# Performance work log

Measured on AMD Instinct MI355X. Metric: run time of the kernel, lower is better.

The kernel has to match this reference:

```python
import jax, jax.numpy as jnp
import numpy as np

B, N, K, CIN, COUT, H = 4, 2048, 32, 16, 32, 32
EPS = 1e-5


def setup_inputs() -> dict:
    key = jax.random.key(0)
    ks = jax.random.split(key, 6)
    s = 0.1
    return dict(
        xyz=jax.random.uniform(ks[0], (B, N, 3), dtype=jnp.float32),
        points=jax.random.normal(ks[1], (B, N, CIN), dtype=jnp.float32),
        W1=jax.random.normal(ks[2], (3, H), dtype=jnp.float32) * s,
        b1=jnp.zeros((H,), jnp.float32),
        g1=jnp.ones((H,), jnp.float32),
        be1=jnp.zeros((H,), jnp.float32),
        W2=jax.random.normal(ks[3], (H, H), dtype=jnp.float32) * s,
        b2=jnp.zeros((H,), jnp.float32),
        g2=jnp.ones((H,), jnp.float32),
        be2=jnp.zeros((H,), jnp.float32),
        W3=jax.random.normal(ks[4], (H, CIN * COUT), dtype=jnp.float32) * s,
        b3=jnp.zeros((CIN * COUT,), jnp.float32),
        gbn=jnp.ones((COUT,), jnp.float32),
        bbn=jnp.zeros((COUT,), jnp.float32),
    )


def _bn(h, g, b):
    # BatchNorm1d training-mode math: biased batch stats over axis 0
    return g * (h - h.mean(0)) / jnp.sqrt(h.var(0) + EPS) + b


def reference(xyz, points, W1, b1, g1, be1, W2, b2, g2, be2, W3, b3, gbn, bbn):
    # KNN: squared distances (B,N,N)
    sq = jnp.sum(xyz * xyz, -1)
    dist = -2.0 * jnp.einsum('bmc,bnc->bmn', xyz, xyz) + sq[:, :, None] + sq[:, None, :]
    _, idx = jax.lax.top_k(-dist, K)  # (B,N,K) nearest neighbors

    gather = jax.vmap(lambda p, i: p[i])  # (N,C),(N,K)->(N,K,C), vmapped over B
    grouped_xyz = gather(xyz, idx)                      # (B,N,K,3)
    rel = grouped_xyz - xyz[:, :, None, :]              # (B,N,K,3)
    grouped_pts = gather(points, idx)                   # (B,N,K,CIN)

    # weight net on relative coords
    h = rel.reshape(-1, 3)
    h = _bn(jax.nn.relu(h @ W1 + b1), g1, be1)
    h = _bn(jax.nn.relu(h @ W2 + b2), g2, be2)
    w = (h @ W3 + b3).reshape(B, N, K, CIN, COUT)       # (B,N,K,CIN,COUT)

    # weighted sum over C_in, then max over neighbors
    out = jnp.einsum('bnkc,bnkco->bnko', grouped_pts, w)  # (B,N,K,COUT)
    out = out.max(axis=2)                                 # (B,N,COUT)

    # final BatchNorm1d over (B,N) per channel
    m = out.mean((0, 1))
    v = out.var((0, 1))
    return gbn * (out - m) / jnp.sqrt(v + EPS) + bbn
```

## Files before the change

### kernel.cpp

```cpp
#include <hip/hip_runtime.h>

#define B_ 4
#define N_ 2048
#define K_ 32
#define CIN_ 16
#define COUT_ 32
#define H_ 32
#define R_ (B_*N_*K_)
#define EPS_ 1e-5f
#define INVR_ (1.0f/(float)R_)
#define INVBN_ (1.0f/(float)(B_*N_))
#define LISTCAP 192
#define NSH 16

typedef __attribute__((ext_vector_type(8)))  _Float16 f16x8;
typedef __attribute__((ext_vector_type(2)))  __fp16   hw16x2;
typedef __attribute__((ext_vector_type(2)))  _Float16 f16x2;
typedef __attribute__((ext_vector_type(16))) float    f32x16;

__device__ __forceinline__ float dot3f(float ax,float ay,float az,float bx,float by,float bz){
    return fmaf(az,bz, fmaf(ay,by, ax*bx));
}
__device__ __forceinline__ unsigned int flip_f32(float d){
    unsigned int u = __float_as_uint(d);
    return u ^ ((unsigned int)(((int)u) >> 31) | 0x80000000u);
}
__device__ __forceinline__ unsigned int pk2(float a, float b){
    union { hw16x2 v; unsigned int u; } c;
    c.v = __builtin_amdgcn_cvt_pkrtz(a, b);
    return c.u;
}
__device__ __forceinline__ unsigned int pkmul(unsigned int a, unsigned int b){
    union { unsigned int u; f16x2 v; } x, y, r;
    x.u = a; y.u = b; r.v = x.v * y.v; return r.u;
}
__device__ __forceinline__ float shsum(const float* __restrict__ p, int k){
    float s = 0.f;
    #pragma unroll
    for (int i = 0; i < NSH; ++i) s += p[i*32 + k];
    return s;
}

__device__ __forceinline__ void hsel4(const unsigned int* hq , int lane,
                                      unsigned int Kthr, int* Bsel, unsigned int* below){
    unsigned int g[4];
    #pragma unroll
    for (int t = 0; t < 4; ++t){
        uint4 h = ((const uint4*)hq)[4*lane + t];
        g[t] = h.x + h.y + h.z + h.w;
    }
    unsigned int gs = g[0]+g[1]+g[2]+g[3], cum = gs;
    #pragma unroll
    for (int off = 1; off < 64; off <<= 1){
        unsigned int v = __shfl_up(cum, off);
        if (lane >= off) cum += v;
    }
    unsigned long long bal = __ballot(cum >= Kthr);
    int L = __ffsll(bal) - 1;
    unsigned int run = __shfl(cum, L) - __shfl(gs, L);
    unsigned int h0 = __shfl(g[0], L), h1 = __shfl(g[1], L), h2 = __shfl(g[2], L);
    if      (run + h0 >= Kthr)           { *Bsel = 4*L;     *below = run; }
    else if (run + h0 + h1 >= Kthr)      { *Bsel = 4*L + 1; *below = run + h0; }
    else if (run + h0 + h1 + h2 >= Kthr) { *Bsel = 4*L + 2; *below = run + h0 + h1; }
    else                                 { *Bsel = 4*L + 3; *below = run + h0 + h1 + h2; }
}

__global__ __launch_bounds__(256) void k_prep0(const float* __restrict__ xyz, float4* __restrict__ xs4g,
                                               float* __restrict__ st){
    int i = blockIdx.x*256 + threadIdx.x;
    float x = xyz[3*i], y = xyz[3*i+1], z = xyz[3*i+2];
    xs4g[i] = make_float4(x, y, z, dot3f(x,y,z,x,y,z));
    if (blockIdx.x == 0){
        for (int j = threadIdx.x; j < 1152; j += 256) st[j] = 0.f;
    }
}

__global__ __launch_bounds__(256,4) void k_knn(const float4* __restrict__ xs4g,
                                               const float* __restrict__ W1, const float* __restrict__ b1,
                                               int* __restrict__ idx_out,
                                               float* __restrict__ s1sh, float* __restrict__ q1sh){
    __shared__ uint4 hist4[4][256];
    __shared__ unsigned long long lst[4][LISTCAP];
    __shared__ int kidx[4][K_];

    const int tid  = threadIdx.x;
    const int w    = tid >> 6;
    const int lane = tid & 63;
    const int half = lane >> 5;
    const int b    = blockIdx.x >> 9;
    const int q    = ((blockIdx.x & 511) << 2) + w;
    const int bN   = b * N_;
    unsigned int* hw = (unsigned int*)hist4[w];

    const uint4 z4 = make_uint4(0,0,0,0);
    hist4[w][lane] = z4; hist4[w][64+lane] = z4; hist4[w][128+lane] = z4; hist4[w][192+lane] = z4;

    const float4 qp = xs4g[bN + q];
    const float qx = qp.x, qy = qp.y, qz = qp.z, sqq = qp.w;

    unsigned int fv[32];
    #pragma unroll
    for (int j = 0; j < 32; ++j){
        int c = j*64 + lane;
        float4 pt = xs4g[bN + c];
        float d = fmaf(-2.0f, dot3f(qx,qy,qz, pt.x,pt.y,pt.z), sqq) + pt.w;
        unsigned int f = flip_f32(d);
        fv[j] = f;
        atomicAdd(&hw[(f >> 24)*4 + (lane & 3)], 1u);
    }
    int B0; unsigned int lt0;
    hsel4(hw, lane, (unsigned)K_, &B0, &lt0);
    unsigned int Kp = (unsigned)K_ - lt0;

    hist4[w][lane] = z4; hist4[w][64+lane] = z4; hist4[w][128+lane] = z4; hist4[w][192+lane] = z4;
    #pragma unroll
    for (int j = 0; j < 32; ++j){
        if ((int)(fv[j] >> 24) == B0)
            atomicAdd(&hw[((fv[j] >> 16) & 0xFF)*4 + (lane & 3)], 1u);
    }
    int B1s; unsigned int lt1;
    hsel4(hw, lane, Kp, &B1s, &lt1);

    const unsigned long long mlt = (lane == 63) ? ~0ull >> 1 : (1ull << lane) - 1ull;
    unsigned int cnt = 0;
    #pragma unroll
    for (int j = 0; j < 32; ++j){
        unsigned int f = fv[j];
        int top = (int)(f >> 24);
        bool surv = (top < B0) || (top == B0 && (int)((f >> 16) & 0xFF) <= B1s);
        unsigned long long sb = __ballot(surv);
        unsigned int pos = cnt + (unsigned int)__popcll(sb & mlt);
        if (surv && pos < (unsigned)LISTCAP)
            lst[w][pos] = ((unsigned long long)f << 32) | (unsigned int)(j*64 + lane);
        cnt += (unsigned int)__popcll(sb);
    }
    int m = (int)cnt; if (m > LISTCAP) m = LISTCAP;

    int* outp = idx_out + ((size_t)bN + q) * K_;
    for (int i = lane; i < m; i += 64){
        unsigned long long my = lst[w][i];
        int rank = 0;
        for (int jj = 0; jj < m; ++jj)
            rank += (lst[w][jj] < my) ? 1 : 0;
        if (rank < K_){
            int id = (int)(unsigned int)(my & 0xFFFFFFFFull);
            outp[rank] = id;
            kidx[w][rank] = id;
        }
    }

    {
        const int ch = lane & 31;
        float w1a = W1[ch], w1b = W1[H_+ch], w1c = W1[2*H_+ch], b1c = b1[ch];
        float s = 0.f, qq = 0.f;
        #pragma unroll
        for (int r = 0; r < 16; ++r){
            int idr = kidx[w][half*16 + r];
            float4 pn = xs4g[bN + idr];
            float rx = pn.x - qx, ry = pn.y - qy, rz = pn.z - qz;
            float h = fmaxf(fmaf(rx, w1a, fmaf(ry, w1b, fmaf(rz, w1c, b1c))), 0.0f);
            s += h; qq = fmaf(h, h, qq);
        }
        s  += __shfl_xor(s, 32, 64);
        qq += __shfl_xor(qq, 32, 64);
        if (lane < 32){
            int sh = (blockIdx.x & (NSH-1)) * 32 + ch;
            atomicAdd(&s1sh[sh], s);
            atomicAdd(&q1sh[sh], qq);
        }
    }
}

__device__ __forceinline__ void compute_h1v(const float4* __restrict__ xs4g, const int* __restrict__ idx, int r,
                                            const float* __restrict__ W1, const float* __restrict__ b1, float* h1){
    int b = r >> 16;
    int n = (r >> 5) & (N_-1);
    int id = idx[r];
    float4 pc = xs4g[b*N_ + n];
    float4 pn = xs4g[b*N_ + id];
    float rx = pn.x - pc.x, ry = pn.y - pc.y, rz = pn.z - pc.z;
    #pragma unroll
    for (int j = 0; j < H_; ++j){
        float a = fmaf(rx, W1[j], fmaf(ry, W1[H_+j], fmaf(rz, W1[2*H_+j], b1[j])));
        h1[j] = fmaxf(a, 0.0f);
    }
}

__global__ __launch_bounds__(256) void k_prep2(const float* __restrict__ points,
                                               const float* __restrict__ s1s, const float* __restrict__ q1s,
                                               const float* __restrict__ g1, const float* __restrict__ be1,
                                               const float* __restrict__ W2, const float* __restrict__ b2,
                                               unsigned int* __restrict__ pf16, unsigned int* __restrict__ W2f,
                                               float* __restrict__ b2p){
    int flat = blockIdx.x*256 + threadIdx.x;
    if (flat < 65536){
        pf16[flat] = pk2(points[2*flat], points[2*flat+1]);
    } else if (flat < 66048){
        int d = flat - 65536;
        int jj = d & 3, lane = (d >> 2) & 63, s = d >> 8;
        int col = lane & 31;
        int k0 = s*16 + (lane >> 5)*8 + 2*jj;
        float m0 = shsum(s1s,k0)*INVR_,   v0 = shsum(q1s,k0)*INVR_   - m0*m0;
        float m1 = shsum(s1s,k0+1)*INVR_, v1 = shsum(q1s,k0+1)*INVR_ - m1*m1;
        float a0  = g1[k0]   / sqrtf(v0 + EPS_);
        float a1v = g1[k0+1] / sqrtf(v1 + EPS_);
        W2f[d] = pk2(a0*W2[k0*H_ + col], a1v*W2[(k0+1)*H_ + col]);
    } else if (flat < 66080){
        int col = flat - 66048;
        float acc = b2[col];
        #pragma unroll 4
        for (int h = 0; h < H_; ++h){
            float mm = shsum(s1s,h)*INVR_, vv = shsum(q1s,h)*INVR_ - mm*mm;
            float aa = g1[h] / sqrtf(vv + EPS_);
            float bb = fmaf(-aa, mm, be1[h]);
            acc = fmaf(bb, W2[h*H_ + col], acc);
        }
        b2p[col] = acc;
    }
}

__global__ __launch_bounds__(256,3) void k_h2stats(const float4* __restrict__ xs4g, const int* __restrict__ idx,
                                                   const float* __restrict__ W1, const float* __restrict__ b1,
                                                   const uint4* __restrict__ W2f, const float* __restrict__ b2p,
                                                   float* gsum, float* gsq){
    __shared__ float redS[H_], redQ[H_];
    const int tid = threadIdx.x, lane = tid & 63, w = tid >> 6;
    const int half = lane >> 5, m = lane & 31;
    if (tid < H_){ redS[tid] = 0.f; redQ[tid] = 0.f; }
    __syncthreads();

    int r = blockIdx.x*256 + tid;
    float h1[H_];
    compute_h1v(xs4g, idx, r, W1, b1, h1);
    unsigned int h1p[16];
    #pragma unroll
    for (int i = 0; i < 16; ++i) h1p[i] = pk2(h1[2*i], h1[2*i+1]);

    union { uint4 u4; f16x8 v; } Bf0, Bf1;
    Bf0.u4 = W2f[lane];
    Bf1.u4 = W2f[64 + lane];
    float b2c = b2p[m];

    float s = 0.f, q = 0.f;
    #pragma unroll
    for (int t = 0; t < 2; ++t){
        const int src = t*32 + m;
        union { unsigned int u[4]; f16x8 v; } a0, a1f;
        #pragma unroll
        for (int jj = 0; jj < 4; ++jj){
            unsigned int lo = __shfl(h1p[jj],     src, 64);
            unsigned int hi = __shfl(h1p[4 + jj], src, 64);
            a0.u[jj] = half ? hi : lo;
        }
        #pragma unroll
        for (int jj = 0; jj < 4; ++jj){
            unsigned int lo = __shfl(h1p[8 + jj],  src, 64);
            unsigned int hi = __shfl(h1p[12 + jj], src, 64);
            a1f.u[jj] = half ? hi : lo;
        }
        f32x16 acc;
        #pragma unroll
        for (int i = 0; i < 16; ++i) acc[i] = b2c;
        acc = __builtin_amdgcn_mfma_f32_32x32x16_f16(a0.v,  Bf0.v, acc, 0, 0, 0);
        acc = __builtin_amdgcn_mfma_f32_32x32x16_f16(a1f.v, Bf1.v, acc, 0, 0, 0);
        #pragma unroll
        for (int i = 0; i < 16; ++i){
            float v = fmaxf(acc[i], 0.0f);
            s += v; q = fmaf(v, v, q);
        }
    }
    s += __shfl_xor(s, 32, 64);
    q += __shfl_xor(q, 32, 64);
    if (lane < 32){ atomicAdd(&redS[m], s); atomicAdd(&redQ[m], q); }
    __syncthreads();
    if (tid < H_){ atomicAdd(&gsum[tid], redS[tid]); atomicAdd(&gsq[tid], redQ[tid]); }
}

__global__ __launch_bounds__(256) void k_prep3(const float* __restrict__ W3, const float* __restrict__ b3,
                                               const float* __restrict__ s2, const float* __restrict__ q2,
                                               const float* __restrict__ g2, const float* __restrict__ be2,
                                               unsigned int* __restrict__ W3f){
    int d = blockIdx.x*256 + threadIdx.x;
    int jj = d & 3, lane = (d >> 2) & 63, step = d >> 8;
    int col = lane & 31;
    int off = (lane >> 5)*8 + 2*jj;
    float v0, v1;
    if (step < 32){
        int h = step, c0 = off;
        float mm = s2[h]*INVR_, vv = q2[h]*INVR_ - mm*mm;
        float aa = g2[h] / sqrtf(vv + EPS_);
        v0 = aa * W3[h*512 + c0*COUT_ + col];
        v1 = aa * W3[h*512 + (c0+1)*COUT_ + col];
    } else {
        int c0 = off;
        v0 = b3[c0*COUT_ + col]; v1 = b3[(c0+1)*COUT_ + col];
        #pragma unroll 4
        for (int h = 0; h < H_; ++h){
            float mm = s2[h]*INVR_, vv = q2[h]*INVR_ - mm*mm;
            float aa = g2[h] / sqrtf(vv + EPS_);
            float bb = fmaf(-aa, mm, be2[h]);
            v0 = fmaf(bb, W3[h*512 + c0*COUT_ + col], v0);
            v1 = fmaf(bb, W3[h*512 + (c0+1)*COUT_ + col], v1);
        }
    }
    W3f[d] = pk2(v0, v1);
}

__global__ __launch_bounds__(256,3) void k_out(const float4* __restrict__ xs4g, const int* __restrict__ idx,
                                               const float* __restrict__ W1, const float* __restrict__ b1,
                                               const uint4* __restrict__ W2f, const float* __restrict__ b2p,
                                               const unsigned int* __restrict__ pf16,
                                               const uint4* __restrict__ W3f,
                                               float* __restrict__ out_pre, float* gsum, float* gsq){
    __shared__ float redS[COUT_], redQ[COUT_];
    const int tid = threadIdx.x, lane = tid & 63, w = tid >> 6;
    const int half = lane >> 5, m = lane & 31;
    if (tid < COUT_){ redS[tid] = 0.f; redQ[tid] = 0.f; }
    __syncthreads();

    const int rB = blockIdx.x*256 + w*64;
    int r = blockIdx.x*256 + tid;

    float h1[H_];
    compute_h1v(xs4g, idx, r, W1, b1, h1);
    unsigned int h1p[16];
    #pragma unroll
    for (int i = 0; i < 16; ++i) h1p[i] = pk2(h1[2*i], h1[2*i+1]);

    union { uint4 u4; f16x8 v; } A0, A1;
    A0.u4 = W2f[lane];
    A1.u4 = W2f[64 + lane];
    float b2v[16];
    #pragma unroll
    for (int i = 0; i < 16; ++i) b2v[i] = b2p[(i&3) + 8*(i>>2) + 4*half];

    const uint4* Wf = W3f + lane;

    #pragma unroll
    for (int t = 0; t < 2; ++t){
        const int src = t*32 + m;
        union { unsigned int u[4]; f16x8 v; } B0f, B1f;
        #pragma unroll
        for (int jj = 0; jj < 4; ++jj){
            unsigned int lo = __shfl(h1p[jj],     src, 64);
            unsigned int hi = __shfl(h1p[4 + jj], src, 64);
            B0f.u[jj] = half ? hi : lo;
        }
        #pragma unroll
        for (int jj = 0; jj < 4; ++jj){
            unsigned int lo = __shfl(h1p[8 + jj],  src, 64);
            unsigned int hi = __shfl(h1p[12 + jj], src, 64);
            B1f.u[jj] = half ? hi : lo;
        }
        f32x16 c2;
        #pragma unroll
        for (int i = 0; i < 16; ++i) c2[i] = b2v[i];
        c2 = __builtin_amdgcn_mfma_f32_32x32x16_f16(A0.v, B0f.v, c2, 0, 0, 0);
        c2 = __builtin_amdgcn_mfma_f32_32x32x16_f16(A1.v, B1f.v, c2, 0, 0, 0);

        unsigned int h2p[16];
        #pragma unroll
        for (int p = 0; p < 8; ++p){
            float v0 = fmaxf(c2[2*p],   0.0f);
            float v1 = fmaxf(c2[2*p+1], 0.0f);
            unsigned int ow = pk2(v0, v1);
            unsigned int ot = __shfl_xor(ow, 32, 64);
            int a = p >> 1, bb = p & 1;
            h2p[4*a + 2*half     + bb] = ow;
            h2p[4*a + 2*(1-half) + bb] = ot;
        }

        int row = rB + t*32 + m;
        int bb_ = row >> 16;
        int idr = idx[row];
        const uint4* gpp = (const uint4*)(pf16 + ((size_t)bb_*N_ + idr)*8);
        uint4 ga = gpp[0], gb = gpp[1];
        unsigned int gsel[4];
        gsel[0] = half ? gb.x : ga.x;
        gsel[1] = half ? gb.y : ga.y;
        gsel[2] = half ? gb.z : ga.z;
        gsel[3] = half ? gb.w : ga.w;

        f32x16 acc;
        #pragma unroll
        for (int i = 0; i < 16; ++i) acc[i] = 0.f;
        #pragma unroll
        for (int kb = 0; kb < 32; ++kb){
            unsigned int hr = h2p[kb >> 1];
            unsigned int hd = __builtin_amdgcn_perm(hr, hr, (kb & 1) ? 0x03020302u : 0x01000100u);
            union { unsigned int u[4]; f16x8 v; } af;
            #pragma unroll
            for (int jj = 0; jj < 4; ++jj) af.u[jj] = pkmul(hd, gsel[jj]);
            union { uint4 u4; f16x8 v; } bf; bf.u4 = Wf[kb*64];
            acc = __builtin_amdgcn_mfma_f32_32x32x16_f16(af.v, bf.v, acc, 0, 0, 0);
        }
        {
            union { unsigned int u[4]; f16x8 v; } af;
            #pragma unroll
            for (int jj = 0; jj < 4; ++jj) af.u[jj] = gsel[jj];
            union { uint4 u4; f16x8 v; } bf; bf.u4 = Wf[32*64];
            acc = __builtin_amdgcn_mfma_f32_32x32x16_f16(af.v, bf.v, acc, 0, 0, 0);
        }

        float v = acc[0];
        #pragma unroll
        for (int i = 1; i < 16; ++i) v = fmaxf(v, acc[i]);
        v = fmaxf(v, __shfl_xor(v, 32, 64));
        if (lane < 32){
            int g = blockIdx.x*8 + w*2 + t;
            out_pre[(size_t)g*COUT_ + m] = v;
            atomicAdd(&redS[m], v);
            atomicAdd(&redQ[m], v*v);
        }
    }
    __syncthreads();
    if (tid < COUT_){ atomicAdd(&gsum[tid], redS[tid]); atomicAdd(&gsq[tid], redQ[tid]); }
}

__global__ __launch_bounds__(256) void k_bn(const float* __restrict__ out_pre,
                                            const float* __restrict__ s3, const float* __restrict__ q3,
                                            const float* __restrict__ gbn, const float* __restrict__ bbn,
                                            float* __restrict__ out){
    int i = blockIdx.x*256 + threadIdx.x;
    int o = i & (COUT_-1);
    float mm = s3[o] * INVBN_;
    float vv = q3[o] * INVBN_ - mm*mm;
    float aa = gbn[o] / sqrtf(vv + EPS_);
    out[i] = fmaf(aa, out_pre[i], fmaf(-aa, mm, bbn[o]));
}

extern "C" void kernel_launch(void* const* d_in, const int* in_sizes, int n_in,
                              void* d_out, int out_size, void* d_ws, size_t ws_size,
                              hipStream_t stream){
    const float* xyz    = (const float*)d_in[0];
    const float* points = (const float*)d_in[1];
    const float* W1  = (const float*)d_in[2];
    const float* b1  = (const float*)d_in[3];
    const float* g1  = (const float*)d_in[4];
    const float* be1 = (const float*)d_in[5];
    const float* W2  = (const float*)d_in[6];
    const float* b2  = (const float*)d_in[7];
    const float* g2  = (const float*)d_in[8];
    const float* be2 = (const float*)d_in[9];
    const float* W3  = (const float*)d_in[10];
    const float* b3  = (const float*)d_in[11];
    const float* gbn = (const float*)d_in[12];
    const float* bbn = (const float*)d_in[13];
    float* out = (float*)d_out;

    char* base = (char*)d_ws;
    int*            idx     = (int*)(base + 0);
    float*          out_pre = (float*)(base + 1048576);
    unsigned int*   pf16    = (unsigned int*)(base + 2097152);
    unsigned int*   W3f     = (unsigned int*)(base + 2359296);
    unsigned int*   W2f     = (unsigned int*)(base + 2393088);
    float*          b2p     = (float*)(base + 2395136);
    float*          st      = (float*)(base + 2395264);
    float4*         xs4g    = (float4*)(base + 2399872);
    float *s1s=st, *q1s=st+512, *s2=st+1024, *q2=st+1056, *s3=st+1088, *q3=st+1120;

    hipLaunchKernelGGL(k_prep0,   dim3(32),      dim3(256), 0, stream, xyz, xs4g, st);
    hipLaunchKernelGGL(k_knn,     dim3(B_*N_/4), dim3(256), 0, stream, xs4g, W1, b1, idx, s1s, q1s);
    hipLaunchKernelGGL(k_prep2,   dim3(260),     dim3(256), 0, stream, points, s1s, q1s, g1, be1, W2, b2,
                       pf16, W2f, b2p);
    hipLaunchKernelGGL(k_h2stats, dim3(R_/256),  dim3(256), 0, stream, xs4g, idx, W1, b1,
                       (const uint4*)W2f, b2p, s2, q2);
    hipLaunchKernelGGL(k_prep3,   dim3(33),      dim3(256), 0, stream, W3, b3, s2, q2, g2, be2, W3f);
    hipLaunchKernelGGL(k_out,     dim3(R_/256),  dim3(256), 0, stream, xs4g, idx, W1, b1,
                       (const uint4*)W2f, b2p, pf16, (const uint4*)W3f, out_pre, s3, q3);
    hipLaunchKernelGGL(k_bn,      dim3(B_*N_*COUT_/256), dim3(256), 0, stream, out_pre, s3, q3, gbn, bbn, out);
}
```

Baseline: 180.4 us.

## Single-pass KNN histogram select, stage W3 in LDS, raise occupancy bounds

KNN selection replaces the two-pass radix histogram with a single 512-bin histogram keyed on the float bits of d+1, which gives a linear-ish distance bucketing. One pass then yields a distance threshold that filters candidates into a smaller list. Separately, k_out copies the W3 fragments (about 33KB) into shared memory per block instead of reading them from global memory per MFMA. Launch bounds are raised for k_knn and k_h2stats. The risks are that distances cluster so that more than LISTCAP candidates survive, which drops true neighbours, and that the larger LDS footprint in k_out limits occupancy.

```diff
diff --git a/kernel.cpp b/kernel.cpp
--- a/kernel.cpp
+++ b/kernel.cpp
@@ -10,7 +10,7 @@
 #define EPS_ 1e-5f
 #define INVR_ (1.0f/(float)R_)
 #define INVBN_ (1.0f/(float)(B_*N_))
-#define LISTCAP 192
+#define LISTCAP 160
 #define NSH 16
 
 typedef __attribute__((ext_vector_type(8)))  _Float16 f16x8;
@@ -21,10 +21,6 @@
 __device__ __forceinline__ float dot3f(float ax,float ay,float az,float bx,float by,float bz){
     return fmaf(az,bz, fmaf(ay,by, ax*bx));
 }
-__device__ __forceinline__ unsigned int flip_f32(float d){
-    unsigned int u = __float_as_uint(d);
-    return u ^ ((unsigned int)(((int)u) >> 31) | 0x80000000u);
-}
 __device__ __forceinline__ unsigned int pk2(float a, float b){
     union { hw16x2 v; unsigned int u; } c;
     c.v = __builtin_amdgcn_cvt_pkrtz(a, b);
@@ -39,30 +35,6 @@
     #pragma unroll
     for (int i = 0; i < NSH; ++i) s += p[i*32 + k];
     return s;
-}
-
-__device__ __forceinline__ void hsel4(const unsigned int* hq , int lane,
-                                      unsigned int Kthr, int* Bsel, unsigned int* below){
-    unsigned int g[4];
-    #pragma unroll
-    for (int t = 0; t < 4; ++t){
-        uint4 h = ((const uint4*)hq)[4*lane + t];
-        g[t] = h.x + h.y + h.z + h.w;
-    }
-    unsigned int gs = g[0]+g[1]+g[2]+g[3], cum = gs;
-    #pragma unroll
-    for (int off = 1; off < 64; off <<= 1){
-        unsigned int v = __shfl_up(cum, off);
-        if (lane >= off) cum += v;
-    }
-    unsigned long long bal = __ballot(cum >= Kthr);
-    int L = __ffsll(bal) - 1;
-    unsigned int run = __shfl(cum, L) - __shfl(gs, L);
-    unsigned int h0 = __shfl(g[0], L), h1 = __shfl(g[1], L), h2 = __shfl(g[2], L);
-    if      (run + h0 >= Kthr)           { *Bsel = 4*L;     *below = run; }
-    else if (run + h0 + h1 >= Kthr)      { *Bsel = 4*L + 1; *below = run + h0; }
-    else if (run + h0 + h1 + h2 >= Kthr) { *Bsel = 4*L + 2; *below = run + h0 + h1; }
-    else                                 { *Bsel = 4*L + 3; *below = run + h0 + h1 + h2; }
 }
 
 __global__ __launch_bounds__(256) void k_prep0(const float* __restrict__ xyz, float4* __restrict__ xs4g,
@@ -75,11 +47,11 @@
     }
 }
 
-__global__ __launch_bounds__(256,4) void k_knn(const float4* __restrict__ xs4g,
+__global__ __launch_bounds__(256,8) void k_knn(const float4* __restrict__ xs4g,
                                                const float* __restrict__ W1, const float* __restrict__ b1,
                                                int* __restrict__ idx_out,
                                                float* __restrict__ s1sh, float* __restrict__ q1sh){
-    __shared__ uint4 hist4[4][256];
+    __shared__ unsigned int hist[4][512][2];
     __shared__ unsigned long long lst[4][LISTCAP];
     __shared__ int kidx[4][K_];
 
@@ -90,10 +62,12 @@
     const int b    = blockIdx.x >> 9;
     const int q    = ((blockIdx.x & 511) << 2) + w;
     const int bN   = b * N_;
-    unsigned int* hw = (unsigned int*)hist4[w];
+    unsigned int* hw = &hist[w][0][0];
 
     const uint4 z4 = make_uint4(0,0,0,0);
-    hist4[w][lane] = z4; hist4[w][64+lane] = z4; hist4[w][128+lane] = z4; hist4[w][192+lane] = z4;
+    uint4* h4 = (uint4*)hw;
+    #pragma unroll
+    for (int i = 0; i < 4; ++i) h4[i*64 + lane] = z4;
 
     const float4 qp = xs4g[bN + q];
     const float qx = qp.x, qy = qp.y, qz = qp.z, sqq = qp.w;
@@ -104,34 +78,55 @@
         int c = j*64 + lane;
         float4 pt = xs4g[bN + c];
         float d = fmaf(-2.0f, dot3f(qx,qy,qz, pt.x,pt.y,pt.z), sqq) + pt.w;
-        unsigned int f = flip_f32(d);
-        fv[j] = f;
-        atomicAdd(&hw[(f >> 24)*4 + (lane & 3)], 1u);
-    }
-    int B0; unsigned int lt0;
-    hsel4(hw, lane, (unsigned)K_, &B0, &lt0);
-    unsigned int Kp = (unsigned)K_ - lt0;
-
-    hist4[w][lane] = z4; hist4[w][64+lane] = z4; hist4[w][128+lane] = z4; hist4[w][192+lane] = z4;
-    #pragma unroll
-    for (int j = 0; j < 32; ++j){
-        if ((int)(fv[j] >> 24) == B0)
-            atomicAdd(&hw[((fv[j] >> 16) & 0xFF)*4 + (lane & 3)], 1u);
-    }
-    int B1s; unsigned int lt1;
-    hsel4(hw, lane, Kp, &B1s, &lt1);
+        fv[j] = __float_as_uint(d);
+        unsigned int u1 = __float_as_uint(d + 1.0f);
+        unsigned int key = (u1 <= 0x3F800000u) ? 0u : ((u1 - 0x3F800000u) >> 15);
+        key = key > 511u ? 511u : key;
+        atomicAdd(&hw[key*2 + (lane & 1)], 1u);
+    }
+
+    unsigned int g[8];
+    #pragma unroll
+    for (int t = 0; t < 4; ++t){
+        uint4 h = ((const uint4*)hw)[lane*4 + t];
+        g[2*t]   = h.x + h.y;
+        g[2*t+1] = h.z + h.w;
+    }
+    unsigned int gs = 0;
+    #pragma unroll
+    for (int t = 0; t < 8; ++t) gs += g[t];
+    unsigned int cum = gs;
+    #pragma unroll
+    for (int off = 1; off < 64; off <<= 1){
+        unsigned int v = __shfl_up(cum, off);
+        if (lane >= off) cum += v;
+    }
+    unsigned long long bal = __ballot(cum >= (unsigned)K_);
+    int L = __ffsll(bal) - 1;
+    unsigned int run = __shfl(cum, L) - __shfl(gs, L);
+    int Bsel = 8*L + 7;
+    {
+        unsigned int c = run; bool fnd = false;
+        #pragma unroll
+        for (int t = 0; t < 8; ++t){
+            unsigned int ht = __shfl(g[t], L, 64);
+            if (!fnd && c + ht >= (unsigned)K_){ Bsel = 8*L + t; fnd = true; }
+            c += ht;
+        }
+    }
+    const float Tedge = __uint_as_float(0x3F800000u + ((unsigned)(Bsel + 1) << 15));
+    const bool allin = (Bsel == 511);
 
     const unsigned long long mlt = (lane == 63) ? ~0ull >> 1 : (1ull << lane) - 1ull;
     unsigned int cnt = 0;
     #pragma unroll
     for (int j = 0; j < 32; ++j){
-        unsigned int f = fv[j];
-        int top = (int)(f >> 24);
-        bool surv = (top < B0) || (top == B0 && (int)((f >> 16) & 0xFF) <= B1s);
+        float f1 = __uint_as_float(fv[j]) + 1.0f;
+        bool surv = (f1 < Tedge) || allin;
         unsigned long long sb = __ballot(surv);
         unsigned int pos = cnt + (unsigned int)__popcll(sb & mlt);
         if (surv && pos < (unsigned)LISTCAP)
-            lst[w][pos] = ((unsigned long long)f << 32) | (unsigned int)(j*64 + lane);
+            lst[w][pos] = ((unsigned long long)fv[j] << 32) | (unsigned int)(j*64 + lane);
         cnt += (unsigned int)__popcll(sb);
     }
     int m = (int)cnt; if (m > LISTCAP) m = LISTCAP;
@@ -219,7 +214,7 @@
     }
 }
 
-__global__ __launch_bounds__(256,3) void k_h2stats(const float4* __restrict__ xs4g, const int* __restrict__ idx,
+__global__ __launch_bounds__(256,4) void k_h2stats(const float4* __restrict__ xs4g, const int* __restrict__ idx,
                                                    const float* __restrict__ W1, const float* __restrict__ b1,
                                                    const uint4* __restrict__ W2f, const float* __restrict__ b2p,
                                                    float* gsum, float* gsq){
@@ -312,9 +307,11 @@
                                                const unsigned int* __restrict__ pf16,
                                                const uint4* __restrict__ W3f,
                                                float* __restrict__ out_pre, float* gsum, float* gsq){
+    __shared__ uint4 Wls[2112];
     __shared__ float redS[COUT_], redQ[COUT_];
     const int tid = threadIdx.x, lane = tid & 63, w = tid >> 6;
     const int half = lane >> 5, m = lane & 31;
+    for (int i = tid; i < 2112; i += 256) Wls[i] = W3f[i];
     if (tid < COUT_){ redS[tid] = 0.f; redQ[tid] = 0.f; }
     __syncthreads();
 
@@ -333,8 +330,6 @@
     float b2v[16];
     #pragma unroll
     for (int i = 0; i < 16; ++i) b2v[i] = b2p[(i&3) + 8*(i>>2) + 4*half];
-
-    const uint4* Wf = W3f + lane;
 
     #pragma unroll
     for (int t = 0; t < 2; ++t){
@@ -391,14 +386,14 @@
             union { unsigned int u[4]; f16x8 v; } af;
             #pragma unroll
             for (int jj = 0; jj < 4; ++jj) af.u[jj] = pkmul(hd, gsel[jj]);
-            union { uint4 u4; f16x8 v; } bf; bf.u4 = Wf[kb*64];
+            union { uint4 u4; f16x8 v; } bf; bf.u4 = Wls[kb*64 + lane];
             acc = __builtin_amdgcn_mfma_f32_32x32x16_f16(af.v, bf.v, acc, 0, 0, 0);
         }
         {
             union { unsigned int u[4]; f16x8 v; } af;
             #pragma unroll
             for (int jj = 0; jj < 4; ++jj) af.u[jj] = gsel[jj];
-            union { uint4 u4; f16x8 v; } bf; bf.u4 = Wf[32*64];
+            union { uint4 u4; f16x8 v; } bf; bf.u4 = Wls[32*64 + lane];
             acc = __builtin_amdgcn_mfma_f32_32x32x16_f16(af.v, bf.v, acc, 0, 0, 0);
         }
 
```

New measurement: 172.3 us. -4.5%, faster.
